# Kernel optimization log

Measured on AMD Instinct MI355X. Metric: run time of the kernel, lower is better.

Reference implementation:

```python
import jax, jax.numpy as jnp
import numpy as np

PAST = 12
FUTURE = 12
INPUT_SIZE = 256
OUTPUT_SIZE = FUTURE * INPUT_SIZE  # 3072


def setup_inputs() -> dict:
    key = jax.random.key(0)
    k_inp, k_w, k_b = jax.random.split(key, 3)
    inp = jax.random.normal(k_inp, (64, 288, INPUT_SIZE), dtype=jnp.float32)
    fan_in = INPUT_SIZE * PAST
    bound = 1.0 / np.sqrt(fan_in)
    # torch nn.Linear init: U(-1/sqrt(fan_in), 1/sqrt(fan_in)); W is (out, in)
    W = jax.random.uniform(k_w, (OUTPUT_SIZE, fan_in), minval=-bound, maxval=bound, dtype=jnp.float32)
    b = jax.random.uniform(k_b, (OUTPUT_SIZE,), minval=-bound, maxval=bound, dtype=jnp.float32)
    return {"inp": inp, "W": W, "b": b}


def reference(inp, W, b):
    batch, length, dim = inp.shape
    n_win = length - PAST  # number of sliding windows (torch loop count)
    # Gather all overlapping windows at once: (batch, n_win, PAST, dim)
    idx = jnp.arange(n_win)[:, None] + jnp.arange(PAST)[None, :]
    windows = inp[:, idx, :].reshape(batch, n_win, PAST * dim)
    # One batched GEMM replaces n_win tiny Linear calls: x @ W.T + b
    out = jnp.einsum('bnk,ok->bno', windows, W) + b
    return out.reshape(batch, -1, FUTURE, dim)
```

## Files before the change

### kernel.cpp

```cpp
#include <hip/hip_runtime.h>
#include <hip/hip_bf16.h>

#define BATCH   64
#define LEN     288
#define DIM     256
#define PAST    12
#define NWIN    (LEN - PAST)
#define M_DIM   (BATCH * NWIN)
#define K_DIM   (PAST * DIM)
#define N_DIM   3072

#define BM 256
#define BN 256
#define BK 64
#define NTILE   (K_DIM / BK)
#define NITER   (NTILE / 2)
#define GRID_M  (M_DIM / BM)
#define GRID_N  (N_DIM / BN)

typedef __attribute__((ext_vector_type(8))) short bh8;
typedef __attribute__((ext_vector_type(4))) float f32x4;

__device__ __forceinline__ void llds16(const void* g, void* l) {
    __builtin_amdgcn_global_load_lds(
        (const __attribute__((address_space(1))) unsigned int*)g,
        (__attribute__((address_space(3))) unsigned int*)l,
        16, 0, 0);
}

__global__ void cvt_f32_bf16(const float* __restrict__ in,
                             __hip_bfloat16* __restrict__ out, int n8) {
    int i = blockIdx.x * blockDim.x + threadIdx.x;
    if (i >= n8) return;
    const float4* p = (const float4*)in;
    float4 a = p[2 * i], b = p[2 * i + 1];
    union { __hip_bfloat16 h[8]; int4 v; } u;
    u.h[0] = __float2bfloat16(a.x); u.h[1] = __float2bfloat16(a.y);
    u.h[2] = __float2bfloat16(a.z); u.h[3] = __float2bfloat16(a.w);
    u.h[4] = __float2bfloat16(b.x); u.h[5] = __float2bfloat16(b.y);
    u.h[6] = __float2bfloat16(b.z); u.h[7] = __float2bfloat16(b.w);
    ((int4*)out)[i] = u.v;
}


#define LDS_A(buf) (smem + (buf) * 65536)
#define LDS_B(buf) (smem + (buf) * 65536 + 32768)

#define PH_MID  __builtin_amdgcn_sched_barrier(0); __builtin_amdgcn_s_barrier(); \
                __builtin_amdgcn_sched_barrier(0); __builtin_amdgcn_s_setprio(1);
#define PH_END  __builtin_amdgcn_s_setprio(0); __builtin_amdgcn_sched_barrier(0); \
                __builtin_amdgcn_s_barrier(); __builtin_amdgcn_sched_barrier(0);
#define PH_END_VM __builtin_amdgcn_s_setprio(0); __builtin_amdgcn_sched_barrier(0); \
                asm volatile("s_waitcnt vmcnt(2)" ::: "memory"); \
                __builtin_amdgcn_s_barrier(); __builtin_amdgcn_sched_barrier(0);

#define RD_A4(buf, MB) { \
    const char* _b = LDS_A(buf) + aRowB; \
    _Pragma("unroll") for (int mi = 0; mi < 4; ++mi) { \
        a0[mi][0] = *(const bh8*)(_b + (MB + mi) * 2048 + kOff0); \
        a0[mi][1] = *(const bh8*)(_b + (MB + mi) * 2048 + kOff1); \
    } }
#define RD_B2(buf, dst, NB) { \
    const char* _b = LDS_B(buf) + bRowB; \
    _Pragma("unroll") for (int ni = 0; ni < 2; ++ni) { \
        dst[ni][0] = *(const bh8*)(_b + (NB + ni) * 2048 + kOff0); \
        dst[ni][1] = *(const bh8*)(_b + (NB + ni) * 2048 + kOff1); \
    } }
#define MFMA_Q(MB, NB, BB) \
    _Pragma("unroll") for (int mi = 0; mi < 4; ++mi) \
    _Pragma("unroll") for (int ni = 0; ni < 2; ++ni) { \
        acc[MB + mi][NB + ni] = __builtin_amdgcn_mfma_f32_16x16x32_bf16( \
            a0[mi][0], BB[ni][0], acc[MB + mi][NB + ni], 0, 0, 0); \
        acc[MB + mi][NB + ni] = __builtin_amdgcn_mfma_f32_16x16x32_bf16( \
            a0[mi][1], BB[ni][1], acc[MB + mi][NB + ni], 0, 0, 0); \
    }
#define STG_A2(buf, kt, h) { \
    llds16(Ag + aSrc[2 * (h)]     + (kt) * 64, LDS_A(buf) + (2 * (h)) * 8192 + wOff); \
    llds16(Ag + aSrc[2 * (h) + 1] + (kt) * 64, LDS_A(buf) + (2 * (h) + 1) * 8192 + wOff); }
#define STG_B2(buf, kt, h) { \
    llds16(Wg + bSrc[2 * (h)]     + (kt) * 64, LDS_B(buf) + (2 * (h)) * 8192 + wOff); \
    llds16(Wg + bSrc[2 * (h) + 1] + (kt) * 64, LDS_B(buf) + (2 * (h) + 1) * 8192 + wOff); }

__global__ __launch_bounds__(512, 2)
void gemm_win8(const __hip_bfloat16* __restrict__ Ag,
               const __hip_bfloat16* __restrict__ Wg,
               const float* __restrict__ bias,
               float* __restrict__ C)
{
    extern __shared__ char smem[];

    const int tid  = threadIdx.x;
    const int nwg = GRID_M * GRID_N;
    const int q = nwg >> 3, r = nwg & 7;
    const int xcd = blockIdx.x & 7, loc = blockIdx.x >> 3;
    const int wgid = (xcd < r ? xcd * (q + 1) : r * (q + 1) + (xcd - r) * q) + loc;
    const int bm = wgid / GRID_N;
    const int bn = wgid - bm * GRID_N;
    const int tile_m = bm * BM;
    const int tile_n = bn * BN;

    const int rd  = tid >> 3;
    const int ch  = tid & 7;
    const int chs = ((ch ^ (rd & 7)) * 8);
    int aSrc[4], bSrc[4];
#pragma unroll
    for (int rb = 0; rb < 4; ++rb) {
        int m  = tile_m + rb * 64 + rd;
        int bq = m / NWIN;
        int wq = m - bq * NWIN;
        aSrc[rb] = (bq * LEN + wq) * DIM + chs;
        bSrc[rb] = (tile_n + rb * 64 + rd) * K_DIM + chs;
    }

    const int wave = tid >> 6, lane = tid & 63;
    const int wm = wave >> 2, wn = wave & 3;
    const int fr = lane & 15, kg = lane >> 4;
    const int sw    = (fr & 7) << 4;
    const int kOff0 = (kg * 16) ^ sw;
    const int kOff1 = kOff0 ^ 64;
    const int aRowB = (wm * 128 + fr) * 128;
    const int bRowB = (wn * 64 + fr) * 128;
    const int wOff  = wave * 1024;

    bh8 a0[4][2], fb0[2][2], fb1[2][2];
    f32x4 acc[8][4] = {};

    STG_A2(0, 0, 0); STG_A2(0, 0, 1); STG_B2(0, 0, 0); STG_B2(0, 0, 1);
    STG_A2(1, 1, 0);
    asm volatile("s_waitcnt vmcnt(2)" ::: "memory");
    __builtin_amdgcn_s_barrier();
    __builtin_amdgcn_sched_barrier(0);

#pragma unroll 1
    for (int it = 0; it < NITER; ++it) {
        const int t1 = 2 * it + 1;
        int t2 = 2 * it + 2; if (t2 >= NTILE) t2 = NTILE - 2;
        int t3 = 2 * it + 3; if (t3 >= NTILE) t3 = NTILE - 1;

        RD_A4(0, 0); RD_B2(0, fb0, 0);
        STG_A2(1, t1, 1);
        PH_MID; MFMA_Q(0, 0, fb0); PH_END;

        RD_B2(0, fb1, 2);
        STG_B2(1, t1, 0);
        PH_MID; MFMA_Q(0, 2, fb1); PH_END;

        RD_A4(0, 4);
        STG_B2(1, t1, 1);
        PH_MID; MFMA_Q(4, 2, fb1); PH_END;

        STG_A2(0, t2, 0);
        PH_MID; MFMA_Q(4, 0, fb0); PH_END_VM;

        RD_A4(1, 0); RD_B2(1, fb0, 0);
        STG_A2(0, t2, 1);
        PH_MID; MFMA_Q(0, 0, fb0); PH_END;

        RD_B2(1, fb1, 2);
        STG_B2(0, t2, 0);
        PH_MID; MFMA_Q(0, 2, fb1); PH_END;

        RD_A4(1, 4);
        STG_B2(0, t2, 1);
        PH_MID; MFMA_Q(4, 2, fb1); PH_END;

        STG_A2(1, t3, 0);
        PH_MID; MFMA_Q(4, 0, fb0); PH_END_VM;
    }

    float bv[4];
    const float* bp = bias + tile_n + wn * 64 + fr;
#pragma unroll
    for (int ni = 0; ni < 4; ++ni) bv[ni] = bp[ni * 16];

    const int r0 = (lane >> 4) * 4;
#pragma unroll
    for (int mi = 0; mi < 8; ++mi) {
#pragma unroll
        for (int j = 0; j < 4; ++j) {
            long m = tile_m + wm * 128 + mi * 16 + r0 + j;
            float* crow = C + m * (long)N_DIM + tile_n + wn * 64 + fr;
#pragma unroll
            for (int ni = 0; ni < 4; ++ni)
                crow[ni * 16] = acc[mi][ni][j] + bv[ni];
        }
    }
}

extern "C" void kernel_launch(void* const* d_in, const int* in_sizes, int n_in,
                              void* d_out, int out_size, void* d_ws, size_t ws_size,
                              hipStream_t stream) {
    const float* inp  = (const float*)d_in[0];
    const float* Wf   = (const float*)d_in[1];
    const float* bias = (const float*)d_in[2];
    float* out = (float*)d_out;

    __hip_bfloat16* Abf = (__hip_bfloat16*)d_ws;
    __hip_bfloat16* Wbf = (__hip_bfloat16*)((char*)d_ws + (size_t)BATCH * LEN * DIM * 2);

    const int nA8 = BATCH * LEN * DIM / 8;
    const int nW8 = N_DIM * K_DIM / 8;
    cvt_f32_bf16<<<(nA8 + 255) / 256, 256, 0, stream>>>(inp, Abf, nA8);
    cvt_f32_bf16<<<(nW8 + 255) / 256, 256, 0, stream>>>(Wf, Wbf, nW8);

    hipFuncSetAttribute((const void*)gemm_win8,
                        hipFuncAttributeMaxDynamicSharedMemorySize, 131072);
    gemm_win8<<<dim3(GRID_M * GRID_N), 512, 131072, stream>>>(Abf, Wbf, bias, out);
}
```

Before: 337.6 us.

## Issue LDS prefetch loads earlier and interleave them across phases with deeper vmcnt

```diff
diff --git a/kernel.cpp b/kernel.cpp
--- a/kernel.cpp
+++ b/kernel.cpp
@@ -47,11 +47,13 @@
 #define LDS_B(buf) (smem + (buf) * 65536 + 32768)
 
 #define PH_MID  __builtin_amdgcn_sched_barrier(0); __builtin_amdgcn_s_barrier(); \
+                __builtin_amdgcn_sched_barrier(0); \
+                asm volatile("s_waitcnt lgkmcnt(0)" ::: "memory"); \
                 __builtin_amdgcn_sched_barrier(0); __builtin_amdgcn_s_setprio(1);
 #define PH_END  __builtin_amdgcn_s_setprio(0); __builtin_amdgcn_sched_barrier(0); \
                 __builtin_amdgcn_s_barrier(); __builtin_amdgcn_sched_barrier(0);
 #define PH_END_VM __builtin_amdgcn_s_setprio(0); __builtin_amdgcn_sched_barrier(0); \
-                asm volatile("s_waitcnt vmcnt(2)" ::: "memory"); \
+                asm volatile("s_waitcnt vmcnt(6)" ::: "memory"); \
                 __builtin_amdgcn_s_barrier(); __builtin_amdgcn_sched_barrier(0);
 
 #define RD_A4(buf, MB) { \
@@ -74,12 +76,10 @@
         acc[MB + mi][NB + ni] = __builtin_amdgcn_mfma_f32_16x16x32_bf16( \
             a0[mi][1], BB[ni][1], acc[MB + mi][NB + ni], 0, 0, 0); \
     }
-#define STG_A2(buf, kt, h) { \
-    llds16(Ag + aSrc[2 * (h)]     + (kt) * 64, LDS_A(buf) + (2 * (h)) * 8192 + wOff); \
-    llds16(Ag + aSrc[2 * (h) + 1] + (kt) * 64, LDS_A(buf) + (2 * (h) + 1) * 8192 + wOff); }
-#define STG_B2(buf, kt, h) { \
-    llds16(Wg + bSrc[2 * (h)]     + (kt) * 64, LDS_B(buf) + (2 * (h)) * 8192 + wOff); \
-    llds16(Wg + bSrc[2 * (h) + 1] + (kt) * 64, LDS_B(buf) + (2 * (h) + 1) * 8192 + wOff); }
+#define STG_A1(buf, kt, q) \
+    llds16(Ag + aSrc[q] + (kt) * 64, LDS_A(buf) + (q) * 8192 + wOff);
+#define STG_B1(buf, kt, u) \
+    llds16(Wg + bSrc[u] + (kt) * 64, LDS_B(buf) + (u) * 8192 + wOff);
 
 __global__ __launch_bounds__(512, 2)
 void gemm_win8(const __hip_bfloat16* __restrict__ Ag,
@@ -100,8 +100,8 @@
     const int tile_n = bn * BN;
 
     const int rd  = tid >> 3;
-    const int ch  = tid & 7;
-    const int chs = ((ch ^ (rd & 7)) * 8);
+    const int ch  = tid & 3 ? (tid & 7) : (tid & 7);
+    const int chs = (((tid & 7) ^ (rd & 7)) * 8);
     int aSrc[4], bSrc[4];
 #pragma unroll
     for (int rb = 0; rb < 4; ++rb) {
@@ -111,6 +111,7 @@
         aSrc[rb] = (bq * LEN + wq) * DIM + chs;
         bSrc[rb] = (tile_n + rb * 64 + rd) * K_DIM + chs;
     }
+    (void)ch;
 
     const int wave = tid >> 6, lane = tid & 63;
     const int wm = wave >> 2, wn = wave & 3;
@@ -125,46 +126,49 @@
     bh8 a0[4][2], fb0[2][2], fb1[2][2];
     f32x4 acc[8][4] = {};
 
-    STG_A2(0, 0, 0); STG_A2(0, 0, 1); STG_B2(0, 0, 0); STG_B2(0, 0, 1);
-    STG_A2(1, 1, 0);
-    asm volatile("s_waitcnt vmcnt(2)" ::: "memory");
+    STG_A1(0, 0, 0); STG_A1(0, 0, 1); STG_A1(0, 0, 2); STG_A1(0, 0, 3);
+    STG_B1(0, 0, 0); STG_B1(0, 0, 1); STG_B1(0, 0, 2); STG_B1(0, 0, 3);
+    STG_A1(1, 1, 0); STG_A1(1, 1, 2);
+    STG_B1(1, 1, 0); STG_B1(1, 1, 1);
+    STG_A1(1, 1, 1); STG_A1(1, 1, 3);
+    asm volatile("s_waitcnt vmcnt(6)" ::: "memory");
     __builtin_amdgcn_s_barrier();
     __builtin_amdgcn_sched_barrier(0);
 
 #pragma unroll 1
     for (int it = 0; it < NITER; ++it) {
-        const int t1 = 2 * it + 1;
-        int t2 = 2 * it + 2; if (t2 >= NTILE) t2 = NTILE - 2;
-        int t3 = 2 * it + 3; if (t3 >= NTILE) t3 = NTILE - 1;
+        const int b = 2 * it + 1;
+        int c = 2 * it + 2; if (c >= NTILE) c = NTILE - 2;
+        int d = 2 * it + 3; if (d >= NTILE) d = NTILE - 1;
 
         RD_A4(0, 0); RD_B2(0, fb0, 0);
-        STG_A2(1, t1, 1);
+        STG_B1(1, b, 2); STG_B1(1, b, 3);
         PH_MID; MFMA_Q(0, 0, fb0); PH_END;
 
         RD_B2(0, fb1, 2);
-        STG_B2(1, t1, 0);
+        STG_A1(0, c, 0); STG_A1(0, c, 2);
         PH_MID; MFMA_Q(0, 2, fb1); PH_END;
 
         RD_A4(0, 4);
-        STG_B2(1, t1, 1);
+        STG_B1(0, c, 0); STG_B1(0, c, 1);
         PH_MID; MFMA_Q(4, 2, fb1); PH_END;
 
-        STG_A2(0, t2, 0);
+        STG_A1(0, c, 1); STG_A1(0, c, 3);
         PH_MID; MFMA_Q(4, 0, fb0); PH_END_VM;
 
         RD_A4(1, 0); RD_B2(1, fb0, 0);
-        STG_A2(0, t2, 1);
+        STG_B1(0, c, 2); STG_B1(0, c, 3);
         PH_MID; MFMA_Q(0, 0, fb0); PH_END;
 
         RD_B2(1, fb1, 2);
-        STG_B2(0, t2, 0);
+        STG_A1(1, d, 0); STG_A1(1, d, 2);
         PH_MID; MFMA_Q(0, 2, fb1); PH_END;
 
         RD_A4(1, 4);
-        STG_B2(0, t2, 1);
+        STG_B1(1, d, 0); STG_B1(1, d, 1);
         PH_MID; MFMA_Q(4, 2, fb1); PH_END;
 
-        STG_A2(1, t3, 0);
+        STG_A1(1, d, 1); STG_A1(1, d, 3);
         PH_MID; MFMA_Q(4, 0, fb0); PH_END_VM;
     }
 
```

New measurement: 340.8 us. No clear change (+0.9%).
